# Kernel tuning notes

Measured on AMD Instinct MI355X. Metric: run time of the kernel, lower is better.

The kernel has to match this reference:

```python
import jax, jax.numpy as jnp
import numpy as np

INPUT_SIZE = 1024
HIDDEN_SIZE = 1024
BATCH = 8192


def setup_inputs() -> dict:
    key = jax.random.key(0)
    ks = jax.random.split(key, 14)
    stdv = 1.0 / HIDDEN_SIZE ** 0.5
    u = lambda k, shape: jax.random.uniform(k, shape, jnp.float32, -stdv, stdv)
    H, I = HIDDEN_SIZE, INPUT_SIZE
    return {
        "x": jax.random.normal(ks[0], (BATCH, I), jnp.float32),
        "hidden": jax.random.normal(ks[1], (BATCH, H), jnp.float32),
        "weight_xr": u(ks[2], (H, I)),
        "weight_hr": u(ks[3], (H, H)),
        "bias_r": u(ks[4], (H,)),
        "weight_xz": u(ks[5], (H, I)),
        "weight_hz": u(ks[6], (H, H)),
        "bias_z": u(ks[7], (H,)),
        "weight_xh": u(ks[8], (H, I)),
        "weight_hh": u(ks[9], (H, H)),
        "bias_h": u(ks[10], (H,)),
        "weight_c": u(ks[11], (H, I + H)),
        "bias_c": u(ks[12], (H,)),
        "weight_hat_h": u(ks[13], (H, I + H)),
        "bias_hat_h": u(jax.random.fold_in(key, 99), (H,)),
    }


def reference(x, hidden, weight_xr, weight_hr, bias_r, weight_xz, weight_hz, bias_z,
              weight_xh, weight_hh, bias_h, weight_c, bias_c, weight_hat_h, bias_hat_h):
    # combined: [B, I+H]
    combined = jnp.concatenate([x, hidden], axis=1)
    c_t = combined @ weight_c.T + bias_c                      # [B, H]
    a_t = jax.nn.softmax(c_t, axis=1)
    hat_h_t = a_t * jax.nn.relu(combined @ weight_hat_h.T + bias_hat_h)
    r_t = jax.nn.sigmoid(x @ weight_xr.T + bias_r + hidden @ weight_hr.T)
    z_t = jax.nn.sigmoid(x @ weight_xz.T + bias_z + hidden @ weight_hz.T)
    h_tilde = jnp.tanh(x @ weight_xh.T + bias_h + (r_t * hidden) @ weight_hh.T)
    h_t = (1.0 - z_t) * h_tilde + z_t * hidden + hat_h_t
    return h_t
```

## Files before the change

kernel.cpp:

```cpp
#include <hip/hip_runtime.h>

typedef unsigned short ushort_t;
typedef __attribute__((ext_vector_type(8))) short short8;
typedef __attribute__((ext_vector_type(4))) float float4v;
typedef __attribute__((ext_vector_type(4))) ushort_t ushort4v;

#define B_ROWS 8192
#define HDIM   1024
#define GLD    5120

__device__ __forceinline__ float bf2f(ushort_t u) {
    return __uint_as_float(((unsigned)u) << 16);
}
__device__ __forceinline__ ushort_t f2bf(float f) {
    unsigned u = __float_as_uint(f);
    u += 0x7FFFu + ((u >> 16) & 1u);
    return (ushort_t)(u >> 16);
}

__global__ __launch_bounds__(256) void pack_all(
    const float* __restrict__ x, const float* __restrict__ h,
    const float* __restrict__ wc, const float* __restrict__ what,
    const float* __restrict__ wxr, const float* __restrict__ whr,
    const float* __restrict__ wxz, const float* __restrict__ whz,
    const float* __restrict__ wxh, const float* __restrict__ whh,
    ushort_t* __restrict__ A, ushort_t* __restrict__ W,
    ushort_t* __restrict__ Whh)
{
    const int bid = blockIdx.x;
    float4v v;
    ushort_t* dst;
    size_t i4;
    if (bid < 16384) {
        i4 = ((size_t)bid * 256 + threadIdx.x) * 4;
        int c = (int)(i4 & 2047);
        size_t b = i4 >> 11;
        const float* src = (c < 1024) ? (x + b * 1024 + c)
                                      : (h + b * 1024 + (c - 1024));
        v = *(const float4v*)src;
        dst = A + i4;
    } else if (bid < 26624) {
        i4 = ((size_t)(bid - 16384) * 256 + threadIdx.x) * 4;
        int j = (int)(i4 >> 11);
        int k = (int)(i4 & 2047);
        int r = j >> 10, jr = j & 1023;
        if (r == 0) {
            v = *(const float4v*)(wc + (size_t)j * 2048 + k);
        } else if (r == 1) {
            v = *(const float4v*)(what + (size_t)jr * 2048 + k);
        } else if (r == 4) {
            v = (k < 1024) ? *(const float4v*)(wxh + (size_t)jr * 1024 + k)
                           : (float4v){0.f, 0.f, 0.f, 0.f};
        } else {
            const float* p0 = (r == 2) ? wxr : wxz;
            const float* p1 = (r == 2) ? whr : whz;
            const float* p = (k < 1024) ? (p0 + (size_t)jr * 1024 + k)
                                        : (p1 + (size_t)jr * 1024 + (k - 1024));
            v = *(const float4v*)p;
        }
        dst = W + i4;
    } else {
        i4 = ((size_t)(bid - 26624) * 256 + threadIdx.x) * 4;
        v = *(const float4v*)(whh + i4);
        dst = Whh + i4;
    }
    ushort4v o;
#pragma unroll
    for (int t = 0; t < 4; ++t) o[t] = f2bf(v[t]);
    *(ushort4v*)dst = o;
}


#define GLOAD(gp, lp) __builtin_amdgcn_global_load_lds( \
    (const __attribute__((address_space(1))) void*)(gp), \
    (__attribute__((address_space(3))) void*)(lp), 16, 0, 0)

#define BARRIER do { __builtin_amdgcn_s_barrier(); \
    __builtin_amdgcn_sched_barrier(0); } while (0)
#define WLG do { \
    asm volatile("s_waitcnt lgkmcnt(0)" ::: "memory"); \
    __builtin_amdgcn_sched_barrier(0); } while (0)
#define WVM(N) do { \
    asm volatile("s_waitcnt vmcnt(" #N ")" ::: "memory"); \
    __builtin_amdgcn_sched_barrier(0); } while (0)

#define STAGE_A(S, H, KT) do { \
    GLOAD(A + (aO0 + (H) * 262144u + (unsigned)(KT) * 64u), \
          dstA + (S) * 32768 + (H) * 8192); \
    GLOAD(A + (aO0 + 16384u + (H) * 262144u + (unsigned)(KT) * 64u), \
          dstA + (S) * 32768 + (H) * 8192 + 512); } while (0)
#define STAGE_B(S, H, KT) do { \
    GLOAD(B + (bO0 + (H) * 262144u + (unsigned)(KT) * 64u), \
          dstB + (S) * 32768 + (H) * 8192); \
    GLOAD(B + (bO0 + 16384u + (H) * 262144u + (unsigned)(KT) * 64u), \
          dstB + (S) * 32768 + (H) * 8192 + 512); } while (0)

#define RD_A4(BK, S, H, KH) do { \
    _Pragma("unroll") \
    for (int mi = 0; mi < 4; ++mi) \
        BK[mi] = *(const short8*)(lds + (S) * 32768 + (H) * 8192 + mi * 1024 \
                                  + ((KH) ? Ard1 : Ard0)); } while (0)

#define RD_B2(BK, S, H, KH) do { \
    _Pragma("unroll") \
    for (int ni = 0; ni < 2; ++ni) \
        BK[ni] = *(const short8*)(lds + 16384 + (S) * 32768 + (H) * 8192 + ni * 1024 \
                                  + ((KH) ? Brd1 : Brd0)); } while (0)

#define MM8(HA, HB, AB, BB) do { \
    __builtin_amdgcn_s_setprio(1); \
    _Pragma("unroll") \
    for (int mi = 0; mi < 4; ++mi) { \
        _Pragma("unroll") \
        for (int ni = 0; ni < 2; ++ni) \
            acc[HA][HB][mi][ni] = __builtin_amdgcn_mfma_f32_16x16x32_bf16( \
                AB[mi], BB[ni], acc[HA][HB][mi][ni], 0, 0, 0); } \
    __builtin_amdgcn_s_setprio(0); } while (0)

__global__ __launch_bounds__(512, 2) void gemm1(
    const ushort_t* __restrict__ A, const ushort_t* __restrict__ B,
    ushort_t* __restrict__ C)
{
    const int bid = blockIdx.x;
    int bx, by;
    if (bid < 512) { int hI = (bid & 7) * 64 + (bid >> 3); by = hI >> 4; bx = hI & 15; }
    else           { int b = bid - 512; int lI = (b & 7) * 16 + (b >> 3); by = lI >> 2; bx = 16 + (lI & 3); }
    const int bn0 = bx * 256;
    const int bm0 = by * 256;
    const int K = (bx >= 16) ? 1024 : 2048;
    const int NIT = K >> 7;

    __shared__ ushort_t lds[65536];

    const int t = threadIdx.x;
    const int w = t >> 6, lane = t & 63;
    const int q = lane >> 4, r16 = lane & 15;

    const int c0 = ((q ^ (r16 & 7)) << 3);
    const int c1 = (((4 + q) ^ (r16 & 7)) << 3);
    const int Ard0 = ((w >> 2) * 64 + r16) * 64 + c0;
    const int Ard1 = ((w >> 2) * 64 + r16) * 64 + c1;
    const int Brd0 = ((w & 3) * 32 + r16) * 64 + c0;
    const int Brd1 = ((w & 3) * 32 + r16) * 64 + c1;

    const unsigned srow0 = (unsigned)(w * 16 + ((lane >> 3) & 7));
    const unsigned kcO = (unsigned)(((lane & 7) ^ (lane >> 3)) << 3);
    const unsigned aO0 = ((unsigned)bm0 + srow0) * 2048u + kcO;
    const unsigned bO0 = ((unsigned)bn0 + srow0) * 2048u + kcO;
    ushort_t* dstA = lds + w * 1024;
    ushort_t* dstB = lds + 16384 + w * 1024;

    float4v acc[2][2][4][2];
#pragma unroll
    for (int i = 0; i < 2; ++i)
#pragma unroll
        for (int j = 0; j < 2; ++j)
#pragma unroll
            for (int m = 0; m < 4; ++m)
#pragma unroll
                for (int n = 0; n < 2; ++n)
                    acc[i][j][m][n] = {0.f, 0.f, 0.f, 0.f};

    short8 X[4], Y[4];
    short8 U[2], V[2];

    STAGE_B(0, 0, 0);
    STAGE_A(0, 0, 0);
    STAGE_A(0, 1, 0);
    STAGE_B(0, 1, 0);
    WVM(4);
    BARRIER;
    RD_A4(X, 0, 0, 0);
    RD_B2(U, 0, 0, 0);

#pragma unroll 1
    for (int it = 0; it < NIT - 1; ++it) {
        const int kO  = 2 * it + 1;
        const int kE2 = 2 * it + 2;
        WVM(2); WLG; BARRIER;
        STAGE_B(1, 0, kO);
        RD_A4(Y, 0, 1, 0);
        MM8(0, 0, X, U);
        WVM(2); WLG; BARRIER;
        STAGE_A(1, 0, kO);
        RD_B2(V, 0, 1, 0);
        MM8(1, 0, Y, U);
        WLG; BARRIER;
        STAGE_A(1, 1, kO);
        RD_B2(U, 0, 0, 1);
        MM8(0, 1, X, V);
        WLG; BARRIER;
        STAGE_B(1, 1, kO);
        RD_A4(X, 0, 0, 1);
        MM8(1, 1, Y, V);
        WLG; BARRIER;
        STAGE_B(0, 0, kE2);
        RD_A4(Y, 0, 1, 1);
        MM8(0, 0, X, U);
        WLG; BARRIER;
        STAGE_A(0, 0, kE2);
        RD_B2(V, 0, 1, 1);
        MM8(1, 0, Y, U);
        WVM(10); WLG; BARRIER;
        STAGE_A(0, 1, kE2);
        RD_B2(U, 1, 0, 0);
        MM8(0, 1, X, V);
        WVM(10); WLG; BARRIER;
        STAGE_B(0, 1, kE2);
        RD_A4(X, 1, 0, 0);
        MM8(1, 1, Y, V);
        WVM(10); WLG; BARRIER;
        RD_A4(Y, 1, 1, 0);
        MM8(0, 0, X, U);
        WVM(8); WLG; BARRIER;
        RD_B2(V, 1, 1, 0);
        MM8(1, 0, Y, U);
        WLG; BARRIER;
        RD_B2(U, 1, 0, 1);
        MM8(0, 1, X, V);
        WLG; BARRIER;
        RD_A4(X, 1, 0, 1);
        MM8(1, 1, Y, V);
        WLG; BARRIER;
        RD_A4(Y, 1, 1, 1);
        MM8(0, 0, X, U);
        WLG; BARRIER;
        RD_B2(V, 1, 1, 1);
        MM8(1, 0, Y, U);
        WVM(6); WLG; BARRIER;
        RD_B2(U, 0, 0, 0);
        MM8(0, 1, X, V);
        WVM(4); WLG; BARRIER;
        RD_A4(X, 0, 0, 0);
        MM8(1, 1, Y, V);
    }

    {
        const int kO = 2 * (NIT - 1) + 1;
        WVM(2); WLG; BARRIER;
        STAGE_B(1, 0, kO);
        RD_A4(Y, 0, 1, 0);
        MM8(0, 0, X, U);
        WVM(2); WLG; BARRIER;
        STAGE_A(1, 0, kO);
        RD_B2(V, 0, 1, 0);
        MM8(1, 0, Y, U);
        WLG; BARRIER;
        STAGE_A(1, 1, kO);
        RD_B2(U, 0, 0, 1);
        MM8(0, 1, X, V);
        WLG; BARRIER;
        STAGE_B(1, 1, kO);
        RD_A4(X, 0, 0, 1);
        MM8(1, 1, Y, V);
        WLG; BARRIER;
        RD_A4(Y, 0, 1, 1);
        MM8(0, 0, X, U);
        WLG; BARRIER;
        RD_B2(V, 0, 1, 1);
        MM8(1, 0, Y, U);
        WVM(6); WLG; BARRIER;
        RD_B2(U, 1, 0, 0);
        MM8(0, 1, X, V);
        WVM(4); WLG; BARRIER;
        RD_A4(X, 1, 0, 0);
        MM8(1, 1, Y, V);
        WVM(2); WLG; BARRIER;
        RD_A4(Y, 1, 1, 0);
        MM8(0, 0, X, U);
        WVM(0); WLG; BARRIER;
        RD_B2(V, 1, 1, 0);
        MM8(1, 0, Y, U);
        WLG; BARRIER;
        RD_B2(U, 1, 0, 1);
        MM8(0, 1, X, V);
        WLG; BARRIER;
        RD_A4(X, 1, 0, 1);
        MM8(1, 1, Y, V);
        WLG; BARRIER;
        RD_A4(Y, 1, 1, 1);
        MM8(0, 0, X, U);
        WLG; BARRIER;
        RD_B2(V, 1, 1, 1);
        MM8(1, 0, Y, U);
        WLG; BARRIER;
        MM8(0, 1, X, V);
        WLG; BARRIER;
        MM8(1, 1, Y, V);
    }

    {
        const int wm2 = w >> 2, wn2 = w & 3;
#pragma unroll
        for (int ha = 0; ha < 2; ++ha)
#pragma unroll
            for (int hb = 0; hb < 2; ++hb)
#pragma unroll
                for (int mi = 0; mi < 4; ++mi)
#pragma unroll
                    for (int ni = 0; ni < 2; ++ni)
#pragma unroll
                        for (int reg = 0; reg < 4; ++reg) {
                            int row = bm0 + ha * 128 + wm2 * 64 + mi * 16 + q * 4 + reg;
                            int col = bn0 + hb * 128 + wn2 * 32 + ni * 16 + r16;
                            C[(size_t)row * GLD + col] = f2bf(acc[ha][hb][mi][ni][reg]);
                        }
    }
}

__global__ __launch_bounds__(256) void row_pass(
    ushort_t* __restrict__ G, const float* __restrict__ bias_c,
    const float* __restrict__ bias_hat, const float* __restrict__ bias_r,
    const float* __restrict__ hidden, ushort_t* __restrict__ rh)
{
    const int wave = threadIdx.x >> 6, lane = threadIdx.x & 63;
    const size_t row = (size_t)blockIdx.x * 4 + wave;
    ushort_t* g = G + row * GLD;
    const int c0 = lane * 16;

    float cv[16];
    {
        short8 a = *(const short8*)(g + c0);
        short8 b = *(const short8*)(g + c0 + 8);
#pragma unroll
        for (int i = 0; i < 8; ++i) {
            cv[i]     = bf2f((ushort_t)a[i]) + bias_c[c0 + i];
            cv[8 + i] = bf2f((ushort_t)b[i]) + bias_c[c0 + 8 + i];
        }
    }
    float mx = cv[0];
#pragma unroll
    for (int i = 1; i < 16; ++i) mx = fmaxf(mx, cv[i]);
#pragma unroll
    for (int m = 1; m < 64; m <<= 1) mx = fmaxf(mx, __shfl_xor(mx, m));
    float sum = 0.f;
#pragma unroll
    for (int i = 0; i < 16; ++i) { cv[i] = __expf(cv[i] - mx); sum += cv[i]; }
#pragma unroll
    for (int m = 1; m < 64; m <<= 1) sum += __shfl_xor(sum, m);
    const float inv = 1.0f / sum;

    {
        short8 a = *(const short8*)(g + 1024 + c0);
        short8 b = *(const short8*)(g + 1024 + c0 + 8);
        short8 oa, ob;
#pragma unroll
        for (int i = 0; i < 8; ++i) {
            float ha = bf2f((ushort_t)a[i]) + bias_hat[c0 + i];
            float hb = bf2f((ushort_t)b[i]) + bias_hat[c0 + 8 + i];
            oa[i] = (short)f2bf(cv[i] * inv * fmaxf(ha, 0.f));
            ob[i] = (short)f2bf(cv[8 + i] * inv * fmaxf(hb, 0.f));
        }
        *(short8*)(g + c0) = oa;
        *(short8*)(g + c0 + 8) = ob;
    }

    {
        short8 a = *(const short8*)(g + 2048 + c0);
        short8 b = *(const short8*)(g + 2048 + c0 + 8);
        const float* hp = hidden + row * 1024 + c0;
        short8 oa, ob;
#pragma unroll
        for (int i = 0; i < 8; ++i) {
            float ra = 1.0f / (1.0f + __expf(-(bf2f((ushort_t)a[i]) + bias_r[c0 + i])));
            float rb = 1.0f / (1.0f + __expf(-(bf2f((ushort_t)b[i]) + bias_r[c0 + 8 + i])));
            oa[i] = (short)f2bf(ra * hp[i]);
            ob[i] = (short)f2bf(rb * hp[8 + i]);
        }
        ushort_t* rp = rh + row * 1024 + c0;
        *(short8*)rp = oa;
        *(short8*)(rp + 8) = ob;
    }
}

#define CSTRIDE 132
__global__ __launch_bounds__(256) void gemm2_final(
    const ushort_t* __restrict__ A, const ushort_t* __restrict__ B,
    const ushort_t* __restrict__ G, const float* __restrict__ bias_z,
    const float* __restrict__ bias_h, const float* __restrict__ hidden,
    float* __restrict__ out)
{
    const int bn0 = blockIdx.x * 128;
    const int bm0 = blockIdx.y * 64;

    __shared__ ushort_t smem[64 * CSTRIDE];
    ushort_t* As = smem;
    ushort_t* Bs = smem + 2048;

    const int t = threadIdx.x;
    const int wave = t >> 6, lane = t & 63;
    const int wr = wave >> 1, wcq = wave & 1;
    const int q = lane >> 4, r16 = lane & 15;
    const int lrow = lane >> 2;
    const int lcol = (lane & 3) * 8;

    float4v acc[2][4];
#pragma unroll
    for (int i = 0; i < 2; ++i)
#pragma unroll
        for (int j = 0; j < 4; ++j)
            acc[i][j] = {0.f, 0.f, 0.f, 0.f};

    for (int k0 = 0; k0 < 1024; k0 += 32) {
#pragma unroll
        for (int j = 0; j < 3; ++j) {
            int l = wave * 3 + j;
            if (l < 4) {
                const ushort_t* gp = A + (size_t)(bm0 + l * 16 + lrow) * 1024 + k0 + lcol;
                __builtin_amdgcn_global_load_lds(
                    (const __attribute__((address_space(1))) void*)gp,
                    (__attribute__((address_space(3))) void*)(As + l * 512),
                    16, 0, 0);
            } else {
                const ushort_t* gp = B + (size_t)(bn0 + (l - 4) * 16 + lrow) * 1024 + k0 + lcol;
                __builtin_amdgcn_global_load_lds(
                    (const __attribute__((address_space(1))) void*)gp,
                    (__attribute__((address_space(3))) void*)(Bs + (l - 4) * 512),
                    16, 0, 0);
            }
        }
        __syncthreads();

        short8 af[2], bf[4];
#pragma unroll
        for (int mi = 0; mi < 2; ++mi)
            af[mi] = *(const short8*)&As[(wr * 32 + mi * 16 + r16) * 32 + q * 8];
#pragma unroll
        for (int ni = 0; ni < 4; ++ni)
            bf[ni] = *(const short8*)&Bs[(wcq * 64 + ni * 16 + r16) * 32 + q * 8];
#pragma unroll
        for (int mi = 0; mi < 2; ++mi)
#pragma unroll
            for (int ni = 0; ni < 4; ++ni)
                acc[mi][ni] = __builtin_amdgcn_mfma_f32_16x16x32_bf16(
                    af[mi], bf[ni], acc[mi][ni], 0, 0, 0);
        __syncthreads();
    }

#pragma unroll
    for (int mi = 0; mi < 2; ++mi)
#pragma unroll
        for (int ni = 0; ni < 4; ++ni)
#pragma unroll
            for (int reg = 0; reg < 4; ++reg) {
                int rl = wr * 32 + mi * 16 + q * 4 + reg;
                int cl = wcq * 64 + ni * 16 + r16;
                smem[rl * CSTRIDE + cl] = f2bf(acc[mi][ni][reg]);
            }
    __syncthreads();

    const int colL = t & 127;
    const int gc = bn0 + colL;
    const float bz = bias_z[gc];
    const float bh = bias_h[gc];
    const int rbase = t >> 7;
#pragma unroll 4
    for (int pass = 0; pass < 32; ++pass) {
        const int rowL = pass * 2 + rbase;
        const size_t gr = (size_t)(bm0 + rowL);
        const ushort_t* grow = G + gr * GLD;
        float z = 1.0f / (1.0f + __expf(-(bf2f(grow[3072 + gc]) + bz)));
        float targ = bf2f(grow[4096 + gc]) + bh + bf2f(smem[rowL * CSTRIDE + colL]);
        float th = 1.0f - 2.0f / (__expf(2.0f * targ) + 1.0f);
        out[gr * 1024 + gc] =
            (1.0f - z) * th + z * hidden[gr * 1024 + gc] + bf2f(grow[gc]);
    }
}


extern "C" void kernel_launch(void* const* d_in, const int* in_sizes, int n_in,
                              void* d_out, int out_size, void* d_ws, size_t ws_size,
                              hipStream_t stream)
{
    const float* x        = (const float*)d_in[0];
    const float* hidden   = (const float*)d_in[1];
    const float* wxr      = (const float*)d_in[2];
    const float* whr      = (const float*)d_in[3];
    const float* bias_r   = (const float*)d_in[4];
    const float* wxz      = (const float*)d_in[5];
    const float* whz      = (const float*)d_in[6];
    const float* bias_z   = (const float*)d_in[7];
    const float* wxh      = (const float*)d_in[8];
    const float* whh      = (const float*)d_in[9];
    const float* bias_h   = (const float*)d_in[10];
    const float* wc       = (const float*)d_in[11];
    const float* bias_c   = (const float*)d_in[12];
    const float* what     = (const float*)d_in[13];
    const float* bias_hat = (const float*)d_in[14];
    float* out = (float*)d_out;

    char* ws = (char*)d_ws;
    ushort_t* G     = (ushort_t*)(ws);
    ushort_t* Abf   = (ushort_t*)(ws + 83886080);
    ushort_t* Wbf   = (ushort_t*)(ws + 117440512);
    ushort_t* Whhbf = (ushort_t*)(ws + 138412032);
    ushort_t* rhbf  = (ushort_t*)(ws + 140509184);

    pack_all<<<27648, 256, 0, stream>>>(x, hidden, wc, what, wxr, whr, wxz, whz,
                                        wxh, whh, Abf, Wbf, Whhbf);

    gemm1<<<640, 512, 0, stream>>>(Abf, Wbf, G);

    row_pass<<<B_ROWS / 4, 256, 0, stream>>>(G, bias_c, bias_hat, bias_r, hidden, rhbf);

    gemm2_final<<<dim3(8, 128), 256, 0, stream>>>(rhbf, Whhbf, G, bias_z, bias_h,
                                                  hidden, out);
}
```

Measured before the change: 354.5 us.

## Deepen GEMM prefetch pipeline and halve LDS barriers per k-step

Reworks the main GEMM loop schedule so the prologue preloads two k-stages into LDS, and each stage's A and B halves are staged together two k-steps ahead. The number of workgroup barriers per iteration drops from one per MFMA block to one per pair, with vmcnt waits consolidated. The goal is to hide global-load latency better and cut barrier stalls. In exchange there is more in-flight LDS buffering and a real risk of races if the fewer barriers do not cover every buffer reuse.

```diff
diff --git a/kernel.cpp b/kernel.cpp
--- a/kernel.cpp
+++ b/kernel.cpp
@@ -164,10 +164,14 @@
     short8 X[4], Y[4];
     short8 U[2], V[2];
 
+    STAGE_A(0, 0, 0);
     STAGE_B(0, 0, 0);
-    STAGE_A(0, 0, 0);
     STAGE_A(0, 1, 0);
     STAGE_B(0, 1, 0);
+    STAGE_B(1, 0, 1);
+    STAGE_A(1, 0, 1);
+    STAGE_A(1, 1, 1);
+    STAGE_B(1, 1, 1);
     WVM(4);
     BARRIER;
     RD_A4(X, 0, 0, 0);
@@ -175,117 +179,80 @@
 
 #pragma unroll 1
     for (int it = 0; it < NIT - 1; ++it) {
-        const int kO  = 2 * it + 1;
         const int kE2 = 2 * it + 2;
-        WVM(2); WLG; BARRIER;
-        STAGE_B(1, 0, kO);
-        RD_A4(Y, 0, 1, 0);
-        MM8(0, 0, X, U);
-        WVM(2); WLG; BARRIER;
-        STAGE_A(1, 0, kO);
-        RD_B2(V, 0, 1, 0);
-        MM8(1, 0, Y, U);
-        WLG; BARRIER;
-        STAGE_A(1, 1, kO);
-        RD_B2(U, 0, 0, 1);
+        const int kO2 = 2 * it + 3;
+        WLG; BARRIER;
+        RD_A4(Y, 0, 1, 0); MM8(0, 0, X, U);
+        WLG;
+        RD_B2(V, 0, 1, 0); MM8(1, 0, Y, U);
+        WLG; BARRIER;
+        RD_B2(U, 0, 0, 1); MM8(0, 1, X, V);
+        WLG;
+        RD_A4(X, 0, 0, 1); MM8(1, 1, Y, V);
+        WLG; BARRIER;
+        STAGE_A(0, 0, kE2); STAGE_B(0, 0, kE2);
+        RD_A4(Y, 0, 1, 1); MM8(0, 0, X, U);
+        WLG;
+        RD_B2(V, 0, 1, 1); MM8(1, 0, Y, U);
+        WLG; BARRIER;
+        STAGE_A(0, 1, kE2); STAGE_B(0, 1, kE2);
+        RD_B2(U, 1, 0, 0); MM8(0, 1, X, V);
+        WLG;
+        RD_A4(X, 1, 0, 0); MM8(1, 1, Y, V);
+        WVM(4);
+        WLG; BARRIER;
+        RD_A4(Y, 1, 1, 0); MM8(0, 0, X, U);
+        WLG;
+        RD_B2(V, 1, 1, 0); MM8(1, 0, Y, U);
+        WLG; BARRIER;
+        RD_B2(U, 1, 0, 1); MM8(0, 1, X, V);
+        WLG;
+        RD_A4(X, 1, 0, 1); MM8(1, 1, Y, V);
+        WLG; BARRIER;
+        STAGE_A(1, 0, kO2); STAGE_B(1, 0, kO2);
+        RD_A4(Y, 1, 1, 1); MM8(0, 0, X, U);
+        WLG;
+        RD_B2(V, 1, 1, 1); MM8(1, 0, Y, U);
+        WLG; BARRIER;
+        STAGE_A(1, 1, kO2); STAGE_B(1, 1, kO2);
+        RD_B2(U, 0, 0, 0); MM8(0, 1, X, V);
+        WLG;
+        RD_A4(X, 0, 0, 0); MM8(1, 1, Y, V);
+        WVM(4);
+    }
+
+    {
+        WLG; BARRIER;
+        RD_A4(Y, 0, 1, 0); MM8(0, 0, X, U);
+        WLG;
+        RD_B2(V, 0, 1, 0); MM8(1, 0, Y, U);
+        WLG; BARRIER;
+        RD_B2(U, 0, 0, 1); MM8(0, 1, X, V);
+        WLG;
+        RD_A4(X, 0, 0, 1); MM8(1, 1, Y, V);
+        WLG; BARRIER;
+        RD_A4(Y, 0, 1, 1); MM8(0, 0, X, U);
+        WLG;
+        RD_B2(V, 0, 1, 1); MM8(1, 0, Y, U);
+        WLG; BARRIER;
+        RD_B2(U, 1, 0, 0); MM8(0, 1, X, V);
+        WLG;
+        RD_A4(X, 1, 0, 0); MM8(1, 1, Y, V);
+        WVM(0);
+        WLG; BARRIER;
+        RD_A4(Y, 1, 1, 0); MM8(0, 0, X, U);
+        WLG;
+        RD_B2(V, 1, 1, 0); MM8(1, 0, Y, U);
+        WLG; BARRIER;
+        RD_B2(U, 1, 0, 1); MM8(0, 1, X, V);
+        WLG;
+        RD_A4(X, 1, 0, 1); MM8(1, 1, Y, V);
+        WLG; BARRIER;
+        RD_A4(Y, 1, 1, 1); MM8(0, 0, X, U);
+        WLG;
+        RD_B2(V, 1, 1, 1); MM8(1, 0, Y, U);
+        WLG; BARRIER;
         MM8(0, 1, X, V);
-        WLG; BARRIER;
-        STAGE_B(1, 1, kO);
-        RD_A4(X, 0, 0, 1);
-        MM8(1, 1, Y, V);
-        WLG; BARRIER;
-        STAGE_B(0, 0, kE2);
-        RD_A4(Y, 0, 1, 1);
-        MM8(0, 0, X, U);
-        WLG; BARRIER;
-        STAGE_A(0, 0, kE2);
-        RD_B2(V, 0, 1, 1);
-        MM8(1, 0, Y, U);
-        WVM(10); WLG; BARRIER;
-        STAGE_A(0, 1, kE2);
-        RD_B2(U, 1, 0, 0);
-        MM8(0, 1, X, V);
-        WVM(10); WLG; BARRIER;
-        STAGE_B(0, 1, kE2);
-        RD_A4(X, 1, 0, 0);
-        MM8(1, 1, Y, V);
-        WVM(10); WLG; BARRIER;
-        RD_A4(Y, 1, 1, 0);
-        MM8(0, 0, X, U);
-        WVM(8); WLG; BARRIER;
-        RD_B2(V, 1, 1, 0);
-        MM8(1, 0, Y, U);
-        WLG; BARRIER;
-        RD_B2(U, 1, 0, 1);
-        MM8(0, 1, X, V);
-        WLG; BARRIER;
-        RD_A4(X, 1, 0, 1);
-        MM8(1, 1, Y, V);
-        WLG; BARRIER;
-        RD_A4(Y, 1, 1, 1);
-        MM8(0, 0, X, U);
-        WLG; BARRIER;
-        RD_B2(V, 1, 1, 1);
-        MM8(1, 0, Y, U);
-        WVM(6); WLG; BARRIER;
-        RD_B2(U, 0, 0, 0);
-        MM8(0, 1, X, V);
-        WVM(4); WLG; BARRIER;
-        RD_A4(X, 0, 0, 0);
-        MM8(1, 1, Y, V);
-    }
-
-    {
-        const int kO = 2 * (NIT - 1) + 1;
-        WVM(2); WLG; BARRIER;
-        STAGE_B(1, 0, kO);
-        RD_A4(Y, 0, 1, 0);
-        MM8(0, 0, X, U);
-        WVM(2); WLG; BARRIER;
-        STAGE_A(1, 0, kO);
-        RD_B2(V, 0, 1, 0);
-        MM8(1, 0, Y, U);
-        WLG; BARRIER;
-        STAGE_A(1, 1, kO);
-        RD_B2(U, 0, 0, 1);
-        MM8(0, 1, X, V);
-        WLG; BARRIER;
-        STAGE_B(1, 1, kO);
-        RD_A4(X, 0, 0, 1);
-        MM8(1, 1, Y, V);
-        WLG; BARRIER;
-        RD_A4(Y, 0, 1, 1);
-        MM8(0, 0, X, U);
-        WLG; BARRIER;
-        RD_B2(V, 0, 1, 1);
-        MM8(1, 0, Y, U);
-        WVM(6); WLG; BARRIER;
-        RD_B2(U, 1, 0, 0);
-        MM8(0, 1, X, V);
-        WVM(4); WLG; BARRIER;
-        RD_A4(X, 1, 0, 0);
-        MM8(1, 1, Y, V);
-        WVM(2); WLG; BARRIER;
-        RD_A4(Y, 1, 1, 0);
-        MM8(0, 0, X, U);
-        WVM(0); WLG; BARRIER;
-        RD_B2(V, 1, 1, 0);
-        MM8(1, 0, Y, U);
-        WLG; BARRIER;
-        RD_B2(U, 1, 0, 1);
-        MM8(0, 1, X, V);
-        WLG; BARRIER;
-        RD_A4(X, 1, 0, 1);
-        MM8(1, 1, Y, V);
-        WLG; BARRIER;
-        RD_A4(Y, 1, 1, 1);
-        MM8(0, 0, X, U);
-        WLG; BARRIER;
-        RD_B2(V, 1, 1, 1);
-        MM8(1, 0, Y, U);
-        WLG; BARRIER;
-        MM8(0, 1, X, V);
-        WLG; BARRIER;
         MM8(1, 1, Y, V);
     }
 
```

Result: no change. 360.1 us (+1.6%).
